# Kernel optimization log

Hardware: AMD Instinct MI355X
Metric: run time of the kernel (lower is better)

## Reference

```python
import jax, jax.numpy as jnp
from jax import lax
import numpy as np

DIM = 64
EMB = 48
PATCH = 8


def setup_inputs() -> dict:
    key = jax.random.key(0)
    ks = jax.random.split(key, 8)
    b, H, W = 4, 256, 256
    x = jax.random.normal(ks[0], (b, DIM, H, W), dtype=jnp.float32)
    prior = jax.random.normal(ks[1], (b, 1, EMB * 4), dtype=jnp.float32)
    # nn.Linear(embed_dim*4, dim*2, bias=False): weight [out, in]
    w_kernel = jax.random.normal(ks[2], (DIM * 2, EMB * 4), dtype=jnp.float32) * 0.05
    # Conv2d(dim, dim*6, 1)
    w_hidden = jax.random.normal(ks[3], (DIM * 6, DIM, 1, 1), dtype=jnp.float32) * 0.05
    # Conv2d(dim*6, dim*6, 3, padding=1, groups=dim*3) -> OIHW with I = 6*dim/(3*dim) = 2
    w_dw = jax.random.normal(ks[4], (DIM * 6, 2, 3, 3), dtype=jnp.float32) * 0.05
    # Conv2d(dim*2, dim, 1)
    w_proj = jax.random.normal(ks[5], (DIM, DIM * 2, 1, 1), dtype=jnp.float32) * 0.05
    ln_weight = jnp.ones((DIM * 2,), dtype=jnp.float32)
    ln_bias = jnp.zeros((DIM * 2,), dtype=jnp.float32)
    return {"x": x, "prior": prior, "w_kernel": w_kernel, "w_hidden": w_hidden,
            "w_dw": w_dw, "w_proj": w_proj, "ln_weight": ln_weight, "ln_bias": ln_bias}


def _patchify(t):
    # b c (h p1) (w p2) -> b c h w p1 p2
    b, c, H, W = t.shape
    t = t.reshape(b, c, H // PATCH, PATCH, W // PATCH, PATCH)
    return t.transpose(0, 1, 2, 4, 3, 5)


def _unpatchify(t):
    # b c h w p1 p2 -> b c (h p1) (w p2)
    b, c, h, w, p1, p2 = t.shape
    return t.transpose(0, 1, 2, 4, 3, 5).reshape(b, c, h * p1, w * p2)


def reference(x, prior, w_kernel, w_hidden, w_dw, w_proj, ln_weight, ln_bias):
    # prior modulation (group == 1 path)
    kv = jnp.einsum('blf,kf->blk', prior, w_kernel)[:, 0]  # [b, 2*dim]
    kv1 = kv[:, :DIM, None, None]
    kv2 = kv[:, DIM:, None, None]
    x = x * kv1 + kv2

    # 1x1 conv to hidden (6*dim channels)
    hidden = jnp.einsum('bchw,oc->bohw', x, w_hidden[:, :, 0, 0])

    # depthwise-ish 3x3 grouped conv, groups = 3*dim
    qkv = lax.conv_general_dilated(
        hidden, w_dw, window_strides=(1, 1), padding='SAME',
        feature_group_count=3 * DIM,
        dimension_numbers=('NCHW', 'OIHW', 'NCHW'))
    q, k, v = jnp.split(qkv, 3, axis=1)  # each [b, 2*dim, H, W]

    # frequency-domain correlation on 8x8 patches
    q_f = jnp.fft.rfft2(_patchify(q))
    k_f = jnp.fft.rfft2(_patchify(k))
    out = jnp.fft.irfft2(q_f * k_f, s=(PATCH, PATCH))
    out = _unpatchify(out)

    # WithBias LayerNorm over channel dim (to_3d puts channels last)
    mu = jnp.mean(out, axis=1, keepdims=True)
    var = jnp.mean((out - mu) ** 2, axis=1, keepdims=True)
    out = (out - mu) / jnp.sqrt(var + 1e-5)
    out = out * ln_weight[None, :, None, None] + ln_bias[None, :, None, None]

    # gate with v and project out
    output = v * out
    output = jnp.einsum('bchw,oc->bohw', output, w_proj[:, :, 0, 0])
    return output
```

## Files before the change

### kernel.cpp

```cpp
#include <hip/hip_runtime.h>


#define HW    65536
#define SLAB  64
#define HROWS 66
#define HSZ2  (HROWS*256)
#define QS    16384

__device__ __forceinline__ unsigned short f2bf(float f) {
    unsigned u = __float_as_uint(f);
    u += 0x7FFFu + ((u >> 16) & 1u);
    return (unsigned short)(u >> 16);
}
__device__ __forceinline__ float bflo(unsigned u) { return __uint_as_float(u << 16); }
__device__ __forceinline__ float bfhi(unsigned u) { return __uint_as_float(u & 0xFFFF0000u); }

__global__ void k_prep(const float* __restrict__ prior, const float* __restrict__ wk,
                       const float* __restrict__ wh, const float* __restrict__ wp,
                       float* __restrict__ kv, float* __restrict__ whT, float* __restrict__ wpT) {
    int t = blockIdx.x * 256 + threadIdx.x;
    if (t < 512) {
        int b = t >> 7, k = t & 127;
        const float* p = prior + b * 192;
        const float* w = wk + k * 192;
        float s = 0.f;
        for (int f = 0; f < 192; ++f) s = fmaf(p[f], w[f], s);
        kv[t] = s;
        return;
    }
    t -= 512;
    if (t < 24576) {
        int c = t / 384, o = t - c * 384;
        whT[t] = wh[o * 64 + c];
        return;
    }
    t -= 24576;
    int c = t >> 6, o = t & 63;
    wpT[t] = wp[o * 128 + c];
}

__global__ __launch_bounds__(256, 4) void k2_hidden(const float* __restrict__ x,
    const float* __restrict__ whT, const float* __restrict__ kv,
    unsigned short* __restrict__ hid, int r0) {
    int row = blockIdx.x * 2 + (threadIdx.x >> 7);
    int cp = threadIdx.x & 127;
    int chunk = blockIdx.y;
    int b = blockIdx.z;
    int g = r0 - 1 + row;
    unsigned* hb = (unsigned*)(hid + ((size_t)(b * 384 + chunk * 32)) * HSZ2
                               + row * 256 + cp * 2);
    if (g < 0 || g > 255) {
        #pragma unroll
        for (int j = 0; j < 32; ++j) hb[(size_t)j * (HSZ2 / 2)] = 0u;
        return;
    }
    const float2* xb = (const float2*)(x + (size_t)b * 64 * HW + g * 256 + cp * 2);
    const float* kv1 = kv + b * 128;
    const float* kv2 = kv1 + 64;
    float acc0[32], acc1[32];
    #pragma unroll
    for (int j = 0; j < 32; ++j) { acc0[j] = 0.f; acc1[j] = 0.f; }
    #pragma unroll 4
    for (int c = 0; c < 64; ++c) {
        float2 xv = xb[(size_t)c * (HW / 2)];
        float xp0 = fmaf(xv.x, kv1[c], kv2[c]);
        float xp1 = fmaf(xv.y, kv1[c], kv2[c]);
        const float* wr = whT + c * 384 + chunk * 32;
        #pragma unroll
        for (int j = 0; j < 32; ++j) {
            acc0[j] = fmaf(wr[j], xp0, acc0[j]);
            acc1[j] = fmaf(wr[j], xp1, acc1[j]);
        }
    }
    #pragma unroll
    for (int j = 0; j < 32; ++j)
        hb[(size_t)j * (HSZ2 / 2)] = (unsigned)f2bf(acc0[j]) | ((unsigned)f2bf(acc1[j]) << 16);
}

__global__ __launch_bounds__(256) void k3_dw(const unsigned short* __restrict__ hid,
    const float* __restrict__ wdw, unsigned short* __restrict__ qkv) {
    __shared__ float sIn[2 * 34 * 66];
    int t = threadIdx.x;
    int bid = blockIdx.x;
    int gl = blockIdx.y;
    int b = blockIdx.z;
    int tx = bid & 3, ty = bid >> 2;
    int x0 = tx * 64, y0 = ty * 32;
    const unsigned short* hbase = hid + ((size_t)(b * 384 + 2 * gl)) * HSZ2;
    for (int idx = t; idx < 2 * 34 * 66; idx += 256) {
        int chl = idx >= 2244;
        int rem = idx - chl * 2244;
        int row = rem / 66;
        int col = rem - row * 66;
        int gx = x0 + col - 1;
        float v = 0.f;
        if (gx >= 0 && gx < 256)
            v = bflo((unsigned)hbase[(size_t)chl * HSZ2 + (y0 + row) * 256 + gx]);
        sIn[idx] = v;
    }
    __syncthreads();
    int og = 2 * gl;
    float w0[18], w1[18];
    #pragma unroll
    for (int i = 0; i < 18; ++i) {
        w0[i] = wdw[(size_t)og * 18 + i];
        w1[i] = wdw[(size_t)(og + 1) * 18 + i];
    }
    unsigned short* q0 = qkv + ((size_t)(b * 384 + og)) * QS;
    #pragma unroll
    for (int pp = 0; pp < 4; ++pp) {
        int ly = pp * 8 + (t >> 5);
        int lxp = (t & 31) * 2;
        float a[2][2];
        #pragma unroll
        for (int px = 0; px < 2; ++px) {
            float s0 = 0.f, s1 = 0.f;
            #pragma unroll
            for (int i = 0; i < 2; ++i)
                #pragma unroll
                for (int ky = 0; ky < 3; ++ky)
                    #pragma unroll
                    for (int kx = 0; kx < 3; ++kx) {
                        float v = sIn[i * 2244 + (ly + ky) * 66 + (lxp + px + kx)];
                        s0 = fmaf(w0[i * 9 + ky * 3 + kx], v, s0);
                        s1 = fmaf(w1[i * 9 + ky * 3 + kx], v, s1);
                    }
            a[px][0] = s0; a[px][1] = s1;
        }
        int row = y0 + ly;
        int gx = x0 + lxp;
        int patch = (row >> 3) * 32 + (gx >> 3);
        int off = patch * 64 + (row & 7) * 8 + (gx & 7);
        ((unsigned*)(q0 + off))[0] =
            (unsigned)f2bf(a[0][0]) | ((unsigned)f2bf(a[1][0]) << 16);
        ((unsigned*)(q0 + QS + off))[0] =
            (unsigned)f2bf(a[0][1]) | ((unsigned)f2bf(a[1][1]) << 16);
    }
}

__global__ __launch_bounds__(256, 2) void kC_patch(const unsigned short* __restrict__ qkv,
    const float* __restrict__ wpT, const float* __restrict__ lnw,
    const float* __restrict__ lnb, float* __restrict__ outp, int r0) {
    __shared__ __align__(16) float sBuf[128 * 68];
    __shared__ __align__(16) float sMu[64];
    __shared__ __align__(16) float sRstd[64];
    int t = threadIdx.x;
    int p = blockIdx.x;
    int b = blockIdx.y;
    int c = t & 127;
    int pyh = t >> 7;

    const uint4* gq = (const uint4*)(qkv + ((size_t)(b * 384 + c)) * QS + p * 64);
    const uint4* gk = (const uint4*)(qkv + ((size_t)(b * 384 + 128 + c)) * QS + p * 64);
    float q[64], k[64];
    #pragma unroll
    for (int f = 0; f < 8; ++f) {
        uint4 u = gq[f];
        q[f * 8 + 0] = bflo(u.x); q[f * 8 + 1] = bfhi(u.x);
        q[f * 8 + 2] = bflo(u.y); q[f * 8 + 3] = bfhi(u.y);
        q[f * 8 + 4] = bflo(u.z); q[f * 8 + 5] = bfhi(u.z);
        q[f * 8 + 6] = bflo(u.w); q[f * 8 + 7] = bfhi(u.w);
    }
    #pragma unroll
    for (int s = 0; s < 8; ++s) {
        int r = (s + 4 * pyh) & 7;
        uint4 u = ((const uint4*)gk)[r];
        k[s * 8 + 0] = bflo(u.x); k[s * 8 + 1] = bfhi(u.x);
        k[s * 8 + 2] = bflo(u.y); k[s * 8 + 3] = bfhi(u.y);
        k[s * 8 + 4] = bflo(u.z); k[s * 8 + 5] = bfhi(u.z);
        k[s * 8 + 6] = bflo(u.w); k[s * 8 + 7] = bfhi(u.w);
    }
    float acc[4][8];
    #pragma unroll
    for (int it = 0; it < 4; ++it)
        #pragma unroll
        for (int px = 0; px < 8; ++px) acc[it][px] = 0.f;
    #pragma unroll
    for (int iy = 0; iy < 8; ++iy)
        #pragma unroll
        for (int ix = 0; ix < 8; ++ix) {
            float qv = q[iy * 8 + ix];
            #pragma unroll
            for (int it = 0; it < 4; ++it) {
                int ks = (it - iy) & 7;
                #pragma unroll
                for (int px = 0; px < 8; ++px)
                    acc[it][px] = fmaf(qv, k[ks * 8 + ((px - ix) & 7)], acc[it][px]);
            }
        }
    #pragma unroll
    for (int it = 0; it < 4; ++it) {
        int pix0 = pyh * 32 + it * 8;
        *(float4*)&sBuf[c * 68 + pix0] =
            make_float4(acc[it][0], acc[it][1], acc[it][2], acc[it][3]);
        *(float4*)&sBuf[c * 68 + pix0 + 4] =
            make_float4(acc[it][4], acc[it][5], acc[it][6], acc[it][7]);
    }
    const uint4* gv = (const uint4*)(qkv + ((size_t)(b * 384 + 256 + c)) * QS
                                     + p * 64 + pyh * 32);
    float vv[32];
    #pragma unroll
    for (int f = 0; f < 4; ++f) {
        uint4 u = gv[f];
        vv[f * 8 + 0] = bflo(u.x); vv[f * 8 + 1] = bfhi(u.x);
        vv[f * 8 + 2] = bflo(u.y); vv[f * 8 + 3] = bfhi(u.y);
        vv[f * 8 + 4] = bflo(u.z); vv[f * 8 + 5] = bfhi(u.z);
        vv[f * 8 + 6] = bflo(u.w); vv[f * 8 + 7] = bfhi(u.w);
    }
    float lw = lnw[c], lb = lnb[c];
    __syncthreads();

    {
        int q4 = (t >> 4) & 3;
        int px = (t & 15) | ((t >> 6) << 4);
        float s = 0.f, s2 = 0.f;
        #pragma unroll
        for (int j = 0; j < 32; ++j) {
            float v = sBuf[(q4 * 32 + j) * 68 + px];
            s += v;
            s2 = fmaf(v, v, s2);
        }
        s  += __shfl_xor(s, 16);   s2 += __shfl_xor(s2, 16);
        s  += __shfl_xor(s, 32);   s2 += __shfl_xor(s2, 32);
        if ((t & 48) == 0) {
            float mu = s * (1.f / 128.f);
            float var = s2 * (1.f / 128.f) - mu * mu;
            sMu[px] = mu;
            sRstd[px] = rsqrtf(var + 1e-5f);
        }
    }
    __syncthreads();
    #pragma unroll
    for (int it = 0; it < 4; ++it) {
        int pix0 = pyh * 32 + it * 8;
        float4 ma = *(const float4*)&sMu[pix0];
        float4 mb = *(const float4*)&sMu[pix0 + 4];
        float4 ra = *(const float4*)&sRstd[pix0];
        float4 rb = *(const float4*)&sRstd[pix0 + 4];
        float mus[8] = {ma.x, ma.y, ma.z, ma.w, mb.x, mb.y, mb.z, mb.w};
        float rss[8] = {ra.x, ra.y, ra.z, ra.w, rb.x, rb.y, rb.z, rb.w};
        #pragma unroll
        for (int px = 0; px < 8; ++px) {
            float tv = fmaf((acc[it][px] - mus[px]) * rss[px], lw, lb)
                       * vv[it * 8 + px];
            sBuf[(pix0 + px) * 132 + c] = tv;
        }
    }
    __syncthreads();
    {
        int px = t & 63;
        int og = __builtin_amdgcn_readfirstlane((t >> 6) * 16);
        float po[16];
        #pragma unroll
        for (int j = 0; j < 16; ++j) po[j] = 0.f;
        const float4* tb = (const float4*)&sBuf[px * 132];
        #pragma unroll 4
        for (int k4 = 0; k4 < 32; ++k4) {
            float4 tv = tb[k4];
            const float* w0 = wpT + (k4 * 4 + 0) * 64 + og;
            const float* w1 = wpT + (k4 * 4 + 1) * 64 + og;
            const float* w2 = wpT + (k4 * 4 + 2) * 64 + og;
            const float* w3 = wpT + (k4 * 4 + 3) * 64 + og;
            #pragma unroll
            for (int j = 0; j < 16; ++j)
                po[j] = fmaf(w0[j], tv.x,
                        fmaf(w1[j], tv.y,
                        fmaf(w2[j], tv.z,
                        fmaf(w3[j], tv.w, po[j]))));
        }
        int grow = r0 + (p >> 5) * 8 + (px >> 3);
        int gcol = (p & 31) * 8 + (px & 7);
        float* ob = outp + ((size_t)(b * 64 + og)) * HW + grow * 256 + gcol;
        #pragma unroll
        for (int j = 0; j < 16; ++j) ob[(size_t)j * HW] = po[j];
    }
}

extern "C" void kernel_launch(void* const* d_in, const int* in_sizes, int n_in,
                              void* d_out, int out_size, void* d_ws, size_t ws_size,
                              hipStream_t stream) {
    const float* x     = (const float*)d_in[0];
    const float* prior = (const float*)d_in[1];
    const float* wk    = (const float*)d_in[2];
    const float* wh    = (const float*)d_in[3];
    const float* wdw   = (const float*)d_in[4];
    const float* wp    = (const float*)d_in[5];
    const float* lnw   = (const float*)d_in[6];
    const float* lnb   = (const float*)d_in[7];
    float* out = (float*)d_out;
    float* ws  = (float*)d_ws;

    float* kv  = ws;
    float* whT = ws + 512;
    float* wpT = ws + 512 + 24576;
    unsigned short* hid = (unsigned short*)(ws + 40960);
    unsigned short* qkv = hid + (size_t)4 * 384 * HSZ2;

    k_prep<<<dim3(130), dim3(256), 0, stream>>>(prior, wk, wh, wp, kv, whT, wpT);
    for (int slab = 0; slab < 4; ++slab) {
        int r0 = slab * SLAB;
        k2_hidden<<<dim3(HROWS / 2, 12, 4), dim3(256), 0, stream>>>(x, whT, kv, hid, r0);
        k3_dw<<<dim3(8, 192, 4), dim3(256), 0, stream>>>(hid, wdw, qkv);
        kC_patch<<<dim3(256, 4), dim3(256), 0, stream>>>(qkv, wpT, lnw, lnb, out, r0);
    }
}
```

Measured before the change: 671.5 us.

## Stage modulated input in shared memory and cover all output channels per block

The hidden 1x1 conv kernel now uses one image row and a 64-column strip per block. It loads the modulated input for all 64 channels into shared memory once, and each wave computes 96 output channels in three passes of 32. Before, each block reloaded x from global memory for every 32-channel output chunk, so x was read 12 times. Now it is read once per block. The trade-offs are one pixel per thread instead of two, which halves weight-register reuse per load, 16-bit stores instead of packed 32-bit stores, and added shared-memory traffic plus a barrier.

```diff
diff --git a/kernel.cpp b/kernel.cpp
--- a/kernel.cpp
+++ b/kernel.cpp
@@ -42,39 +42,59 @@
 __global__ __launch_bounds__(256, 4) void k2_hidden(const float* __restrict__ x,
     const float* __restrict__ whT, const float* __restrict__ kv,
     unsigned short* __restrict__ hid, int r0) {
-    int row = blockIdx.x * 2 + (threadIdx.x >> 7);
-    int cp = threadIdx.x & 127;
-    int chunk = blockIdx.y;
+    __shared__ float sXp[64 * 64];
+    int t = threadIdx.x;
+    int row = blockIdx.x;
+    int colq = blockIdx.y;
     int b = blockIdx.z;
+    int col0 = colq * 64;
     int g = r0 - 1 + row;
-    unsigned* hb = (unsigned*)(hid + ((size_t)(b * 384 + chunk * 32)) * HSZ2
-                               + row * 256 + cp * 2);
+    int px = t & 63;
+    int wv = t >> 6;
+    unsigned short* hb = hid + ((size_t)(b * 384 + wv * 96)) * HSZ2
+                         + row * 256 + col0 + px;
     if (g < 0 || g > 255) {
         #pragma unroll
-        for (int j = 0; j < 32; ++j) hb[(size_t)j * (HSZ2 / 2)] = 0u;
+        for (int it = 0; it < 3; ++it)
+            #pragma unroll
+            for (int j = 0; j < 32; ++j)
+                hb[(size_t)(it * 32 + j) * HSZ2] = 0;
         return;
     }
-    const float2* xb = (const float2*)(x + (size_t)b * 64 * HW + g * 256 + cp * 2);
     const float* kv1 = kv + b * 128;
     const float* kv2 = kv1 + 64;
-    float acc0[32], acc1[32];
-    #pragma unroll
-    for (int j = 0; j < 32; ++j) { acc0[j] = 0.f; acc1[j] = 0.f; }
-    #pragma unroll 4
-    for (int c = 0; c < 64; ++c) {
-        float2 xv = xb[(size_t)c * (HW / 2)];
-        float xp0 = fmaf(xv.x, kv1[c], kv2[c]);
-        float xp1 = fmaf(xv.y, kv1[c], kv2[c]);
-        const float* wr = whT + c * 384 + chunk * 32;
-        #pragma unroll
-        for (int j = 0; j < 32; ++j) {
-            acc0[j] = fmaf(wr[j], xp0, acc0[j]);
-            acc1[j] = fmaf(wr[j], xp1, acc1[j]);
-        }
-    }
-    #pragma unroll
-    for (int j = 0; j < 32; ++j)
-        hb[(size_t)j * (HSZ2 / 2)] = (unsigned)f2bf(acc0[j]) | ((unsigned)f2bf(acc1[j]) << 16);
+    const float2* xb = (const float2*)(x + (size_t)b * 64 * HW + (size_t)g * 256 + col0);
+    #pragma unroll
+    for (int i = 0; i < 8; ++i) {
+        int idx = t + i * 256;
+        int c = idx >> 5;
+        int l2 = idx & 31;
+        float2 xv = xb[(size_t)c * (HW / 2) + l2];
+        float2 s;
+        s.x = fmaf(xv.x, kv1[c], kv2[c]);
+        s.y = fmaf(xv.y, kv1[c], kv2[c]);
+        *(float2*)&sXp[c * 64 + l2 * 2] = s;
+    }
+    __syncthreads();
+    #pragma unroll
+    for (int it = 0; it < 3; ++it) {
+        int obase = wv * 96 + it * 32;
+        const float* wbase = whT + obase;
+        float acc[32];
+        #pragma unroll
+        for (int j = 0; j < 32; ++j) acc[j] = 0.f;
+        #pragma unroll 4
+        for (int c = 0; c < 64; ++c) {
+            float xv = sXp[c * 64 + px];
+            const float* wr = wbase + c * 384;
+            #pragma unroll
+            for (int j = 0; j < 32; ++j)
+                acc[j] = fmaf(wr[j], xv, acc[j]);
+        }
+        #pragma unroll
+        for (int j = 0; j < 32; ++j)
+            hb[(size_t)(it * 32 + j) * HSZ2] = f2bf(acc[j]);
+    }
 }
 
 __global__ __launch_bounds__(256) void k3_dw(const unsigned short* __restrict__ hid,
@@ -299,7 +319,7 @@
     k_prep<<<dim3(130), dim3(256), 0, stream>>>(prior, wk, wh, wp, kv, whT, wpT);
     for (int slab = 0; slab < 4; ++slab) {
         int r0 = slab * SLAB;
-        k2_hidden<<<dim3(HROWS / 2, 12, 4), dim3(256), 0, stream>>>(x, whT, kv, hid, r0);
+        k2_hidden<<<dim3(HROWS, 4, 4), dim3(256), 0, stream>>>(x, whT, kv, hid, r0);
         k3_dw<<<dim3(8, 192, 4), dim3(256), 0, stream>>>(hid, wdw, qkv);
         kC_patch<<<dim3(256, 4), dim3(256), 0, stream>>>(qkv, wpT, lnw, lnb, out, r0);
     }
```

Result: slower. 1.329 ms (+97.9%).

## Restructure hidden 1x1 conv with shared-memory staged inputs and narrower output chunks

Applied to the files above, without the earlier changes.

The 1x1 hidden-projection kernel now has each block handle one image row and 24 output channels. The modulated input row is staged into shared memory in two 32-channel passes, and each thread computes one pixel instead of two. This lowers the per-thread register load and produces more blocks. The cost is that each block writes 16-bit values instead of packed 32-bit ones, and input rows are re-read across 16 chunk blocks. The patch kernel's launch bound also changes its occupancy hint from 2 to 3 blocks, which may cause register spills.

```diff
diff --git a/kernel.cpp b/kernel.cpp
--- a/kernel.cpp
+++ b/kernel.cpp
@@ -42,39 +42,53 @@
 __global__ __launch_bounds__(256, 4) void k2_hidden(const float* __restrict__ x,
     const float* __restrict__ whT, const float* __restrict__ kv,
     unsigned short* __restrict__ hid, int r0) {
-    int row = blockIdx.x * 2 + (threadIdx.x >> 7);
-    int cp = threadIdx.x & 127;
-    int chunk = blockIdx.y;
+    __shared__ float sXp[32 * 256];
+    int t = threadIdx.x;
+    int chunk = blockIdx.x;
+    int row = blockIdx.y;
     int b = blockIdx.z;
     int g = r0 - 1 + row;
-    unsigned* hb = (unsigned*)(hid + ((size_t)(b * 384 + chunk * 32)) * HSZ2
-                               + row * 256 + cp * 2);
+    int och0 = chunk * 24;
+    unsigned short* hb = hid + ((size_t)(b * 384 + och0)) * HSZ2 + row * 256 + t;
     if (g < 0 || g > 255) {
         #pragma unroll
-        for (int j = 0; j < 32; ++j) hb[(size_t)j * (HSZ2 / 2)] = 0u;
+        for (int j = 0; j < 24; ++j) hb[(size_t)j * HSZ2] = 0;
         return;
     }
-    const float2* xb = (const float2*)(x + (size_t)b * 64 * HW + g * 256 + cp * 2);
     const float* kv1 = kv + b * 128;
     const float* kv2 = kv1 + 64;
-    float acc0[32], acc1[32];
-    #pragma unroll
-    for (int j = 0; j < 32; ++j) { acc0[j] = 0.f; acc1[j] = 0.f; }
-    #pragma unroll 4
-    for (int c = 0; c < 64; ++c) {
-        float2 xv = xb[(size_t)c * (HW / 2)];
-        float xp0 = fmaf(xv.x, kv1[c], kv2[c]);
-        float xp1 = fmaf(xv.y, kv1[c], kv2[c]);
-        const float* wr = whT + c * 384 + chunk * 32;
-        #pragma unroll
-        for (int j = 0; j < 32; ++j) {
-            acc0[j] = fmaf(wr[j], xp0, acc0[j]);
-            acc1[j] = fmaf(wr[j], xp1, acc1[j]);
-        }
-    }
-    #pragma unroll
-    for (int j = 0; j < 32; ++j)
-        hb[(size_t)j * (HSZ2 / 2)] = (unsigned)f2bf(acc0[j]) | ((unsigned)f2bf(acc1[j]) << 16);
+    const float2* xb = (const float2*)(x + (size_t)b * 64 * HW + (size_t)g * 256);
+    float acc[24];
+    #pragma unroll
+    for (int j = 0; j < 24; ++j) acc[j] = 0.f;
+    #pragma unroll
+    for (int pass = 0; pass < 2; ++pass) {
+        int cbase = pass * 32;
+        #pragma unroll
+        for (int i = 0; i < 16; ++i) {
+            int idx = t + i * 256;
+            int c = idx >> 7;
+            int l2 = idx & 127;
+            float2 xv = xb[(size_t)(cbase + c) * (HW / 2) + l2];
+            float2 s;
+            s.x = fmaf(xv.x, kv1[cbase + c], kv2[cbase + c]);
+            s.y = fmaf(xv.y, kv1[cbase + c], kv2[cbase + c]);
+            *(float2*)&sXp[c * 256 + l2 * 2] = s;
+        }
+        __syncthreads();
+        #pragma unroll 4
+        for (int c = 0; c < 32; ++c) {
+            float xv = sXp[c * 256 + t];
+            const float* wr = whT + (size_t)(cbase + c) * 384 + och0;
+            #pragma unroll
+            for (int j = 0; j < 24; ++j)
+                acc[j] = fmaf(wr[j], xv, acc[j]);
+        }
+        if (pass == 0) __syncthreads();
+    }
+    #pragma unroll
+    for (int j = 0; j < 24; ++j)
+        hb[(size_t)j * HSZ2] = f2bf(acc[j]);
 }
 
 __global__ __launch_bounds__(256) void k3_dw(const unsigned short* __restrict__ hid,
@@ -138,7 +152,7 @@
     }
 }
 
-__global__ __launch_bounds__(256, 2) void kC_patch(const unsigned short* __restrict__ qkv,
+__global__ __launch_bounds__(256, 3) void kC_patch(const unsigned short* __restrict__ qkv,
     const float* __restrict__ wpT, const float* __restrict__ lnw,
     const float* __restrict__ lnb, float* __restrict__ outp, int r0) {
     __shared__ __align__(16) float sBuf[128 * 68];
@@ -299,7 +313,7 @@
     k_prep<<<dim3(130), dim3(256), 0, stream>>>(prior, wk, wh, wp, kv, whT, wpT);
     for (int slab = 0; slab < 4; ++slab) {
         int r0 = slab * SLAB;
-        k2_hidden<<<dim3(HROWS / 2, 12, 4), dim3(256), 0, stream>>>(x, whT, kv, hid, r0);
+        k2_hidden<<<dim3(16, HROWS, 4), dim3(256), 0, stream>>>(x, whT, kv, hid, r0);
         k3_dw<<<dim3(8, 192, 4), dim3(256), 0, stream>>>(hid, wdw, qkv);
         kC_patch<<<dim3(256, 4), dim3(256), 0, stream>>>(qkv, wpT, lnw, lnb, out, r0);
     }
```

New measurement: 755.9 us. +12.6%, slower.
